# Kernel tuning notes

Hardware: AMD Instinct MI355X
Metric: run time of the kernel (lower is better)

Reference implementation:

```python
import jax, jax.numpy as jnp
import numpy as np

N_DATA = 128      # number of datasets (process conditions)
SEG_LEN = 131072  # thickness points per dataset
N_MAT = 8         # number of distinct materials
N_MATP = 8        # material params: Sigma0, BetaD, Ea, Mfda, Di, A0, B0, l0
N_PROCP = 5       # process params: SigmaC, K0, alpha1, L0, GrainSize_200
RGAS = 8.314      # gas constant, J/(mol K)


def setup_inputs() -> dict:
    key = jax.random.key(0)
    k1, k2, k3, k4 = jax.random.split(key, 4)
    # thickness points: sorted within each dataset segment, scaled to [0, 1]
    x = jax.random.uniform(k1, (N_DATA, SEG_LEN), dtype=jnp.float32)
    x_scaled = jnp.sort(x, axis=1).reshape(-1)
    # process conditions [R, T, P, Melting_T]
    pc = jax.random.uniform(k2, (N_DATA, 4), dtype=jnp.float32)
    R = 0.05 + pc[:, 0]            # deposition rate
    T = 300.0 + 300.0 * pc[:, 1]   # temperature (K)
    P = 0.1 + pc[:, 2]             # pressure
    material_index = jnp.sort(jax.random.randint(k3, (N_DATA,), 0, N_MAT, dtype=jnp.int32))
    melting_T = 1000.0 + 100.0 * material_index.astype(jnp.float32)
    process_c = jnp.stack([R, T, P, melting_T], axis=1)
    # learned raw parameters (pre-sigmoid) and bounds
    n_params = N_MAT * N_MATP + N_DATA * N_PROCP  # 704
    raw_params = 0.5 * jax.random.normal(k4, (n_params,), dtype=jnp.float32)
    para_lb = jnp.full((n_params,), 0.1, dtype=jnp.float32)
    para_ub = jnp.full((n_params,), 2.0, dtype=jnp.float32)
    # MinMaxScaler surrogates: [x_data_min, x_data_max, y_data_min, y_data_max], feature_range=(0,1)
    scaler_params = jnp.array([0.5, 500.0, -50.0, 50.0], dtype=jnp.float32)
    fit_index = jnp.repeat(jnp.arange(1, N_DATA + 1, dtype=jnp.int32), SEG_LEN)
    return {
        'x_scaled': x_scaled, 'process_c': process_c, 'raw_params': raw_params,
        'para_lb': para_lb, 'para_ub': para_ub, 'scaler_params': scaler_params,
        'fit_index': fit_index, 'material_index': material_index,
    }


def _stress(tp, R, T, P, SigmaC, alpha1, L0, G200, Sigma0, BetaD, Ea, Mfda, Di, A0, B0, l0):
    """Kinetic stress equation (Chason-type). tp: [N, L-1]; params broadcast [N, 1]."""
    Lg = G200 * (tp / 200.0 + 1e-3) ** alpha1 + L0      # grain size evolution
    D = Di * jnp.exp(-Ea / (RGAS * T))                   # thermally activated diffusivity
    beta = BetaD * D / (R * Lg + 1e-9)                   # kinetic competition factor
    sigma_ss = (SigmaC - Mfda * P + (Sigma0 / Lg) * beta) / (1.0 + beta)
    return sigma_ss + A0 * jnp.exp(-tp / (B0 * l0 + 1e-9))  # steady-state + transient


def reference(x_scaled, process_c, raw_params, para_lb, para_ub, scaler_params,
              fit_index, material_index):
    n_data = process_c.shape[0]
    seg = x_scaled.shape[0] // n_data
    # unscale parameters: sigmoid -> [lb, ub]
    xv = jax.nn.sigmoid(raw_params) * (para_ub - para_lb) + para_lb
    materials = xv[:N_MAT * N_MATP].reshape(N_MAT, N_MATP)
    process = xv[N_MAT * N_MATP:].reshape(n_data, N_PROCP)
    x_min, x_max, y_min, y_max = scaler_params[0], scaler_params[1], scaler_params[2], scaler_params[3]
    # inverse MinMax transform of thickness (feature_range = (0, 1))
    t = (x_scaled * (x_max - x_min) + x_min).reshape(n_data, seg)  # [N, L]
    SigmaC, K0, alpha1, L0, G200 = (process[:, i:i + 1] for i in range(5))
    mat = materials[material_index]  # [N, 8] gather per-dataset material params
    Sigma0, BetaD, Ea, Mfda, Di, A0, B0, l0 = (mat[:, i:i + 1] for i in range(8))
    R, T, P = process_c[:, 0:1], process_c[:, 1:2], process_c[:, 2:3]
    # Euler integration: Fit[j+1] = Fit[j] + stress(t[j]) * dT  ==  K0 + cumsum
    s = _stress(t[:, :-1], R, T, P, SigmaC, alpha1, L0, G200,
                Sigma0, BetaD, Ea, Mfda, Di, A0, B0, l0)   # [N, L-1]
    dT = jnp.diff(t, axis=1)                                # [N, L-1]
    fit = jnp.concatenate([K0, K0 + jnp.cumsum(s * dT, axis=1)], axis=1).reshape(-1)
    # forward MinMax transform of stress-thickness (feature_range = (0, 1))
    return (fit - y_min) / (y_max - y_min)
```

## Files before the change

kernel.cpp:

```cpp
#include <hip/hip_runtime.h>

#define N_DATA   128
#define SEG_LEN  131072
#define NPROD    (SEG_LEN - 1)
#define N_MAT    8
#define N_MATP   8
#define N_PROCP  5
#define RGAS     8.314f

#define TPB      256
#define EPT      16
#define WCHUNK   (64 * EPT)
#define WPR      (SEG_LEN / WCHUNK)
#define NWAVE    (N_DATA * WPR)
#define NBLK     (NWAVE / (TPB / 64))

typedef float nt4 __attribute__((ext_vector_type(4)));

__device__ __forceinline__ float stress_s(float t,
    float alpha1, float L0, float G200, float Sigma0, float A0,
    float inv_tau, float cbd, float base_num, float R) {
  float Lg  = G200 * __expf(alpha1 * __logf(t * (1.0f / 200.0f) + 0.001f)) + L0;
  float u   = R * Lg + 1e-9f;
  float num = base_num * u * Lg + Sigma0 * cbd;
  float den = Lg * (u + cbd);
  float sigma_ss = num * __builtin_amdgcn_rcpf(den);
  return sigma_ss + A0 * __expf(-t * inv_tau);
}

__global__ __launch_bounds__(TPB) void k0_init(unsigned long long* __restrict__ cs) {
  cs[blockIdx.x * TPB + threadIdx.x] = 0ull;
}

__global__ __launch_bounds__(TPB) void k_scan(
    const float* __restrict__ x,
    const float* __restrict__ pc, const float* __restrict__ raw,
    const float* __restrict__ lb, const float* __restrict__ ub,
    const float* __restrict__ sc, const int* __restrict__ mat_idx,
    unsigned long long* __restrict__ cs,
    float* __restrict__ out) {
  int tid  = threadIdx.x;
  int lane = tid & 63;
  int w    = blockIdx.x * (TPB >> 6) + (tid >> 6);
  int row  = __builtin_amdgcn_readfirstlane(w >> 7);
  int s    = w & (WPR - 1);

  long rowbase = (long)row * SEG_LEN;
  int  gbl = s * WCHUNK + lane * EPT;
  const float* xp = x + rowbase + gbl;
  float4 a0 = *(const float4*)(xp);
  float4 a1 = *(const float4*)(xp + 4);
  float4 a2 = *(const float4*)(xp + 8);
  float4 a3 = *(const float4*)(xp + 12);
  float  xn = (gbl + EPT < SEG_LEN) ? xp[EPT] : 0.0f;

  float pvl = 0.0f;
  if (lane < 13) {
    int idx = (lane < 5) ? (N_MAT * N_MATP + row * N_PROCP + lane)
                         : (mat_idx[row] * N_MATP + (lane - 5));
    float sg = 1.0f / (1.0f + __expf(-raw[idx]));
    pvl = sg * (ub[idx] - lb[idx]) + lb[idx];
  }
  float SigmaC = __shfl(pvl, 0),  K0   = __shfl(pvl, 1), alpha1 = __shfl(pvl, 2);
  float L0     = __shfl(pvl, 3),  G200 = __shfl(pvl, 4);
  float Sigma0 = __shfl(pvl, 5),  BetaD = __shfl(pvl, 6), Ea = __shfl(pvl, 7);
  float Mfda   = __shfl(pvl, 8),  Di   = __shfl(pvl, 9);
  float A0     = __shfl(pvl, 10), B0   = __shfl(pvl, 11), l0 = __shfl(pvl, 12);

  float R = pc[row * 4 + 0], T = pc[row * 4 + 1], P = pc[row * 4 + 2];
  float cbd      = BetaD * Di * __expf(-Ea / (RGAS * T));
  float base_num = SigmaC - Mfda * P;
  float inv_tau  = 1.0f / (B0 * l0 + 1e-9f);
  float x_min = sc[0], x_sc = sc[1] - sc[0];
  float y_min = sc[2], inv_yr = 1.0f / (sc[3] - sc[2]);

  float xr[EPT + 1];
  xr[0]=a0.x; xr[1]=a0.y; xr[2]=a0.z; xr[3]=a0.w;
  xr[4]=a1.x; xr[5]=a1.y; xr[6]=a1.z; xr[7]=a1.w;
  xr[8]=a2.x; xr[9]=a2.y; xr[10]=a2.z; xr[11]=a2.w;
  xr[12]=a3.x; xr[13]=a3.y; xr[14]=a3.z; xr[15]=a3.w;
  xr[16]=xn;

  float pref[EPT];
  float run  = 0.0f;
  float tcur = xr[0] * x_sc + x_min;
#pragma unroll
  for (int k = 0; k < EPT; k++) {
    float tnext = xr[k + 1] * x_sc + x_min;
    float p = 0.0f;
    if (gbl + k < NPROD) {
      float ss = stress_s(tcur, alpha1, L0, G200, Sigma0, A0, inv_tau, cbd, base_num, R);
      p = ss * (tnext - tcur);
    }
    run += p;
    pref[k] = run;
    tcur = tnext;
  }

  float incl = run;
#pragma unroll
  for (int d = 1; d < 64; d <<= 1) {
    float n = __shfl_up(incl, d);
    if (lane >= d) incl += n;
  }

  if (lane == 63) {
    unsigned long long u = (1ull << 32) |
        (unsigned long long)__float_as_uint(incl);
    __hip_atomic_store(cs + w, u, __ATOMIC_RELAXED, __HIP_MEMORY_SCOPE_AGENT);
  }

  float v = 0.0f;
  for (int c = lane; c < s; c += 64) {
    const unsigned long long* p = cs + ((row << 7) + c);
    unsigned long long u;
    do {
      u = __hip_atomic_load(p, __ATOMIC_RELAXED, __HIP_MEMORY_SCOPE_AGENT);
    } while (!(unsigned)(u >> 32));
    v += __uint_as_float((unsigned)u);
  }
#pragma unroll
  for (int d = 32; d > 0; d >>= 1) v += __shfl_down(v, d);
  float choff = __shfl(v, 0);

  float base = K0 + choff + (incl - run);
  nt4 o0, o1, o2, o3;
  o0.x = (base            - y_min) * inv_yr;
  o0.y = (base + pref[0]  - y_min) * inv_yr;
  o0.z = (base + pref[1]  - y_min) * inv_yr;
  o0.w = (base + pref[2]  - y_min) * inv_yr;
  o1.x = (base + pref[3]  - y_min) * inv_yr;
  o1.y = (base + pref[4]  - y_min) * inv_yr;
  o1.z = (base + pref[5]  - y_min) * inv_yr;
  o1.w = (base + pref[6]  - y_min) * inv_yr;
  o2.x = (base + pref[7]  - y_min) * inv_yr;
  o2.y = (base + pref[8]  - y_min) * inv_yr;
  o2.z = (base + pref[9]  - y_min) * inv_yr;
  o2.w = (base + pref[10] - y_min) * inv_yr;
  o3.x = (base + pref[11] - y_min) * inv_yr;
  o3.y = (base + pref[12] - y_min) * inv_yr;
  o3.z = (base + pref[13] - y_min) * inv_yr;
  o3.w = (base + pref[14] - y_min) * inv_yr;
  nt4* op = (nt4*)(out + rowbase + gbl);
  __builtin_nontemporal_store(o0, op);
  __builtin_nontemporal_store(o1, op + 1);
  __builtin_nontemporal_store(o2, op + 2);
  __builtin_nontemporal_store(o3, op + 3);
}

extern "C" void kernel_launch(void* const* d_in, const int* in_sizes, int n_in,
                              void* d_out, int out_size, void* d_ws, size_t ws_size,
                              hipStream_t stream) {
  const float* x_scaled  = (const float*)d_in[0];
  const float* process_c = (const float*)d_in[1];
  const float* raw       = (const float*)d_in[2];
  const float* lb        = (const float*)d_in[3];
  const float* ub        = (const float*)d_in[4];
  const float* sc        = (const float*)d_in[5];
  const int*   mat_idx   = (const int*)d_in[7];
  float* out = (float*)d_out;
  unsigned long long* cs = (unsigned long long*)d_ws;

  k0_init<<<NWAVE / TPB, TPB, 0, stream>>>(cs);
  k_scan<<<NBLK, TPB, 0, stream>>>(
      x_scaled, process_c, raw, lb, ub, sc, mat_idx, cs, out);
}
```

Measured before the change: 203.1 us.

## Coalesce wave loads and publish chunk total before local scan

Each lane now reads four float4s strided by 256 floats, so every wave load instruction touches contiguous memory, where before each lane read 16 contiguous floats. Neighbour values come from cross-lane shuffles, and four separate wave scans rebuild the prefix order. The chunk total is found with an xor reduction and published before the local scans, so later waves can stop waiting sooner. Outputs are prepared before the lookback wait, and the spin loop now sleeps between polls. This adds more shuffle work and changes the order of float summation.

Measured after the change: 181.0 us. 10.9% less time.

```diff
diff --git a/kernel.cpp b/kernel.cpp
--- a/kernel.cpp
+++ b/kernel.cpp
@@ -43,16 +43,17 @@
   int lane = tid & 63;
   int w    = blockIdx.x * (TPB >> 6) + (tid >> 6);
   int row  = __builtin_amdgcn_readfirstlane(w >> 7);
-  int s    = w & (WPR - 1);
+  int s    = __builtin_amdgcn_readfirstlane(w & (WPR - 1));
 
   long rowbase = (long)row * SEG_LEN;
-  int  gbl = s * WCHUNK + lane * EPT;
-  const float* xp = x + rowbase + gbl;
-  float4 a0 = *(const float4*)(xp);
-  float4 a1 = *(const float4*)(xp + 4);
-  float4 a2 = *(const float4*)(xp + 8);
-  float4 a3 = *(const float4*)(xp + 12);
-  float  xn = (gbl + EPT < SEG_LEN) ? xp[EPT] : 0.0f;
+  int  gb0 = s * WCHUNK;
+  const float* xp = x + rowbase + gb0 + lane * 4;
+  float4 v0 = *(const float4*)(xp);
+  float4 v1 = *(const float4*)(xp + 256);
+  float4 v2 = *(const float4*)(xp + 512);
+  float4 v3 = *(const float4*)(xp + 768);
+  float  xe = 0.0f;
+  if (lane == 63 && gb0 + WCHUNK < SEG_LEN) xe = x[rowbase + gb0 + WCHUNK];
 
   float pvl = 0.0f;
   if (lane < 13) {
@@ -74,78 +75,113 @@
   float x_min = sc[0], x_sc = sc[1] - sc[0];
   float y_min = sc[2], inv_yr = 1.0f / (sc[3] - sc[2]);
 
-  float xr[EPT + 1];
-  xr[0]=a0.x; xr[1]=a0.y; xr[2]=a0.z; xr[3]=a0.w;
-  xr[4]=a1.x; xr[5]=a1.y; xr[6]=a1.z; xr[7]=a1.w;
-  xr[8]=a2.x; xr[9]=a2.y; xr[10]=a2.z; xr[11]=a2.w;
-  xr[12]=a3.x; xr[13]=a3.y; xr[14]=a3.z; xr[15]=a3.w;
-  xr[16]=xn;
-
-  float pref[EPT];
-  float run  = 0.0f;
-  float tcur = xr[0] * x_sc + x_min;
+  float t0[4] = {v0.x*x_sc+x_min, v0.y*x_sc+x_min, v0.z*x_sc+x_min, v0.w*x_sc+x_min};
+  float t1[4] = {v1.x*x_sc+x_min, v1.y*x_sc+x_min, v1.z*x_sc+x_min, v1.w*x_sc+x_min};
+  float t2[4] = {v2.x*x_sc+x_min, v2.y*x_sc+x_min, v2.z*x_sc+x_min, v2.w*x_sc+x_min};
+  float t3[4] = {v3.x*x_sc+x_min, v3.y*x_sc+x_min, v3.z*x_sc+x_min, v3.w*x_sc+x_min};
+
+  float d0 = __shfl_down(t0[0], 1);
+  float d1 = __shfl_down(t1[0], 1);
+  float d2 = __shfl_down(t2[0], 1);
+  float d3 = __shfl_down(t3[0], 1);
+  float b1 = __shfl(t1[0], 0);
+  float b2 = __shfl(t2[0], 0);
+  float b3 = __shfl(t3[0], 0);
+  float xet = xe * x_sc + x_min;
+  bool last = (lane == 63);
+  float n0 = last ? b1  : d0;
+  float n1 = last ? b2  : d1;
+  float n2 = last ? b3  : d2;
+  float n3 = last ? xet : d3;
+
+  int glb = gb0 + lane * 4;
+  float p0[4], p1[4], p2[4], p3[4];
+#define PROD(pd, td, nd, roff)                                              \
+  {                                                                         \
+    _Pragma("unroll")                                                       \
+    for (int k = 0; k < 4; k++) {                                           \
+      float tn = (k < 3) ? td[k + 1] : nd;                                  \
+      float pp = 0.0f;                                                      \
+      if (glb + (roff) + k < NPROD) {                                       \
+        float ss = stress_s(td[k], alpha1, L0, G200, Sigma0, A0,            \
+                            inv_tau, cbd, base_num, R);                     \
+        pp = ss * (tn - td[k]);                                             \
+      }                                                                     \
+      pd[k] = pp;                                                           \
+    }                                                                       \
+  }
+  PROD(p0, t0, n0, 0)
+  PROD(p1, t1, n1, 256)
+  PROD(p2, t2, n2, 512)
+  PROD(p3, t3, n3, 768)
+#undef PROD
+
+  float rs0 = p0[0]+p0[1]+p0[2]+p0[3];
+  float rs1 = p1[0]+p1[1]+p1[2]+p1[3];
+  float rs2 = p2[0]+p2[1]+p2[2]+p2[3];
+  float rs3 = p3[0]+p3[1]+p3[2]+p3[3];
+
+  float tot = rs0 + rs1 + rs2 + rs3;
 #pragma unroll
-  for (int k = 0; k < EPT; k++) {
-    float tnext = xr[k + 1] * x_sc + x_min;
-    float p = 0.0f;
-    if (gbl + k < NPROD) {
-      float ss = stress_s(tcur, alpha1, L0, G200, Sigma0, A0, inv_tau, cbd, base_num, R);
-      p = ss * (tnext - tcur);
-    }
-    run += p;
-    pref[k] = run;
-    tcur = tnext;
-  }
-
-  float incl = run;
-#pragma unroll
-  for (int d = 1; d < 64; d <<= 1) {
-    float n = __shfl_up(incl, d);
-    if (lane >= d) incl += n;
-  }
-
-  if (lane == 63) {
+  for (int d = 1; d < 64; d <<= 1) tot += __shfl_xor(tot, d);
+  if (lane == 0) {
     unsigned long long u = (1ull << 32) |
-        (unsigned long long)__float_as_uint(incl);
+        (unsigned long long)__float_as_uint(tot);
     __hip_atomic_store(cs + w, u, __ATOMIC_RELAXED, __HIP_MEMORY_SCOPE_AGENT);
   }
 
-  float v = 0.0f;
+  float carry = 0.0f, e0, e1, e2, e3;
+#define SCAN(rs, er)                                                        \
+  {                                                                         \
+    float inc = rs;                                                         \
+    _Pragma("unroll")                                                       \
+    for (int d = 1; d < 64; d <<= 1) {                                      \
+      float nn = __shfl_up(inc, d);                                         \
+      if (lane >= d) inc += nn;                                             \
+    }                                                                       \
+    er = carry + inc - rs;                                                  \
+    carry += __shfl(inc, 63);                                               \
+  }
+  SCAN(rs0, e0) SCAN(rs1, e1) SCAN(rs2, e2) SCAN(rs3, e3)
+#undef SCAN
+
+  nt4 o0, o1, o2, o3;
+#define PREP(od, er, pd)                                                    \
+  {                                                                         \
+    float c0 = K0 + (er)        - y_min;                                    \
+    float c1 = c0 + pd[0];                                                  \
+    float c2 = c1 + pd[1];                                                  \
+    float c3 = c2 + pd[2];                                                  \
+    od.x = c0 * inv_yr; od.y = c1 * inv_yr;                                 \
+    od.z = c2 * inv_yr; od.w = c3 * inv_yr;                                 \
+  }
+  PREP(o0, e0, p0) PREP(o1, e1, p1) PREP(o2, e2, p2) PREP(o3, e3, p3)
+#undef PREP
+
+  float vsum = 0.0f;
   for (int c = lane; c < s; c += 64) {
     const unsigned long long* p = cs + ((row << 7) + c);
-    unsigned long long u;
-    do {
+    unsigned long long u = __hip_atomic_load(p, __ATOMIC_RELAXED, __HIP_MEMORY_SCOPE_AGENT);
+    while (!(unsigned)(u >> 32)) {
+      __builtin_amdgcn_s_sleep(1);
       u = __hip_atomic_load(p, __ATOMIC_RELAXED, __HIP_MEMORY_SCOPE_AGENT);
-    } while (!(unsigned)(u >> 32));
-    v += __uint_as_float((unsigned)u);
+    }
+    vsum += __uint_as_float((unsigned)u);
   }
 #pragma unroll
-  for (int d = 32; d > 0; d >>= 1) v += __shfl_down(v, d);
-  float choff = __shfl(v, 0);
-
-  float base = K0 + choff + (incl - run);
-  nt4 o0, o1, o2, o3;
-  o0.x = (base            - y_min) * inv_yr;
-  o0.y = (base + pref[0]  - y_min) * inv_yr;
-  o0.z = (base + pref[1]  - y_min) * inv_yr;
-  o0.w = (base + pref[2]  - y_min) * inv_yr;
-  o1.x = (base + pref[3]  - y_min) * inv_yr;
-  o1.y = (base + pref[4]  - y_min) * inv_yr;
-  o1.z = (base + pref[5]  - y_min) * inv_yr;
-  o1.w = (base + pref[6]  - y_min) * inv_yr;
-  o2.x = (base + pref[7]  - y_min) * inv_yr;
-  o2.y = (base + pref[8]  - y_min) * inv_yr;
-  o2.z = (base + pref[9]  - y_min) * inv_yr;
-  o2.w = (base + pref[10] - y_min) * inv_yr;
-  o3.x = (base + pref[11] - y_min) * inv_yr;
-  o3.y = (base + pref[12] - y_min) * inv_yr;
-  o3.z = (base + pref[13] - y_min) * inv_yr;
-  o3.w = (base + pref[14] - y_min) * inv_yr;
-  nt4* op = (nt4*)(out + rowbase + gbl);
-  __builtin_nontemporal_store(o0, op);
-  __builtin_nontemporal_store(o1, op + 1);
-  __builtin_nontemporal_store(o2, op + 2);
-  __builtin_nontemporal_store(o3, op + 3);
+  for (int d = 32; d > 0; d >>= 1) vsum += __shfl_down(vsum, d);
+  float choff = __shfl(vsum, 0) * inv_yr;
+
+  o0.x += choff; o0.y += choff; o0.z += choff; o0.w += choff;
+  o1.x += choff; o1.y += choff; o1.z += choff; o1.w += choff;
+  o2.x += choff; o2.y += choff; o2.z += choff; o2.w += choff;
+  o3.x += choff; o3.y += choff; o3.z += choff; o3.w += choff;
+
+  float* ob = out + rowbase + gb0 + lane * 4;
+  __builtin_nontemporal_store(o0, (nt4*)(ob));
+  __builtin_nontemporal_store(o1, (nt4*)(ob + 256));
+  __builtin_nontemporal_store(o2, (nt4*)(ob + 512));
+  __builtin_nontemporal_store(o3, (nt4*)(ob + 768));
 }
 
 extern "C" void kernel_launch(void* const* d_in, const int* in_sizes, int n_in,
```

## Use per-row bitmask lookback and coalesced strided loads with 32 elements per lane

Applied to the files above, without the earlier changes.

Each wave now handles twice as many elements, loaded as coalesced float4 runs strided across lanes, with neighbour values obtained by shuffles instead of per-lane contiguous chunks. Cross-wave offsets move from a polled per-wave flag-plus-value word to a per-row 64-bit ready mask updated with fetch_or and a separate value array, so a wave polls one word, with a short sleep between polls. The intent is better load coalescing, fewer waves and cheaper lookback, at the cost of eight in-wave scans per wave and more contention on the shared mask atomic.

Result: slower. 502.8 us (+147.6%).

```diff
diff --git a/kernel.cpp b/kernel.cpp
--- a/kernel.cpp
+++ b/kernel.cpp
@@ -9,7 +9,8 @@
 #define RGAS     8.314f
 
 #define TPB      256
-#define EPT      16
+#define RUNS     8
+#define EPT      (RUNS * 4)
 #define WCHUNK   (64 * EPT)
 #define WPR      (SEG_LEN / WCHUNK)
 #define NWAVE    (N_DATA * WPR)
@@ -28,8 +29,8 @@
   return sigma_ss + A0 * __expf(-t * inv_tau);
 }
 
-__global__ __launch_bounds__(TPB) void k0_init(unsigned long long* __restrict__ cs) {
-  cs[blockIdx.x * TPB + threadIdx.x] = 0ull;
+__global__ __launch_bounds__(128) void k0_init(unsigned long long* __restrict__ mask) {
+  mask[threadIdx.x] = 0ull;
 }
 
 __global__ __launch_bounds__(TPB) void k_scan(
@@ -37,22 +38,22 @@
     const float* __restrict__ pc, const float* __restrict__ raw,
     const float* __restrict__ lb, const float* __restrict__ ub,
     const float* __restrict__ sc, const int* __restrict__ mat_idx,
-    unsigned long long* __restrict__ cs,
+    unsigned long long* __restrict__ mask, float* __restrict__ val,
     float* __restrict__ out) {
   int tid  = threadIdx.x;
   int lane = tid & 63;
   int w    = blockIdx.x * (TPB >> 6) + (tid >> 6);
-  int row  = __builtin_amdgcn_readfirstlane(w >> 7);
-  int s    = w & (WPR - 1);
+  int row  = __builtin_amdgcn_readfirstlane(w / WPR);
+  int s    = __builtin_amdgcn_readfirstlane(w & (WPR - 1));
 
   long rowbase = (long)row * SEG_LEN;
-  int  gbl = s * WCHUNK + lane * EPT;
-  const float* xp = x + rowbase + gbl;
-  float4 a0 = *(const float4*)(xp);
-  float4 a1 = *(const float4*)(xp + 4);
-  float4 a2 = *(const float4*)(xp + 8);
-  float4 a3 = *(const float4*)(xp + 12);
-  float  xn = (gbl + EPT < SEG_LEN) ? xp[EPT] : 0.0f;
+  int  gb0 = s * WCHUNK;
+  const float* xp = x + rowbase + gb0 + lane * 4;
+  float4 v[RUNS];
+#pragma unroll
+  for (int r = 0; r < RUNS; r++) v[r] = *(const float4*)(xp + r * 256);
+  float xe = 0.0f;
+  if (lane == 63 && gb0 + WCHUNK < SEG_LEN) xe = x[rowbase + gb0 + WCHUNK];
 
   float pvl = 0.0f;
   if (lane < 13) {
@@ -74,78 +75,110 @@
   float x_min = sc[0], x_sc = sc[1] - sc[0];
   float y_min = sc[2], inv_yr = 1.0f / (sc[3] - sc[2]);
 
-  float xr[EPT + 1];
-  xr[0]=a0.x; xr[1]=a0.y; xr[2]=a0.z; xr[3]=a0.w;
-  xr[4]=a1.x; xr[5]=a1.y; xr[6]=a1.z; xr[7]=a1.w;
-  xr[8]=a2.x; xr[9]=a2.y; xr[10]=a2.z; xr[11]=a2.w;
-  xr[12]=a3.x; xr[13]=a3.y; xr[14]=a3.z; xr[15]=a3.w;
-  xr[16]=xn;
-
-  float pref[EPT];
-  float run  = 0.0f;
-  float tcur = xr[0] * x_sc + x_min;
-#pragma unroll
-  for (int k = 0; k < EPT; k++) {
-    float tnext = xr[k + 1] * x_sc + x_min;
-    float p = 0.0f;
-    if (gbl + k < NPROD) {
-      float ss = stress_s(tcur, alpha1, L0, G200, Sigma0, A0, inv_tau, cbd, base_num, R);
-      p = ss * (tnext - tcur);
+  float t[RUNS][4];
+#pragma unroll
+  for (int r = 0; r < RUNS; r++) {
+    t[r][0] = v[r].x * x_sc + x_min;
+    t[r][1] = v[r].y * x_sc + x_min;
+    t[r][2] = v[r].z * x_sc + x_min;
+    t[r][3] = v[r].w * x_sc + x_min;
+  }
+
+  float nx[RUNS];
+  {
+    float dsh[RUNS], bc[RUNS];
+#pragma unroll
+    for (int r = 0; r < RUNS; r++) dsh[r] = __shfl_down(t[r][0], 1);
+#pragma unroll
+    for (int r = 0; r < RUNS - 1; r++) bc[r] = __shfl(t[r + 1][0], 0);
+    bc[RUNS - 1] = xe * x_sc + x_min;
+    bool last = (lane == 63);
+#pragma unroll
+    for (int r = 0; r < RUNS; r++) nx[r] = last ? bc[r] : dsh[r];
+  }
+
+  int glb = gb0 + lane * 4;
+  float rs[RUNS];
+#pragma unroll
+  for (int r = 0; r < RUNS; r++) {
+    float acc = 0.0f;
+#pragma unroll
+    for (int k = 0; k < 4; k++) {
+      float tn = (k < 3) ? t[r][k + 1] : nx[r];
+      float pp = 0.0f;
+      if (glb + r * 256 + k < NPROD) {
+        float ss = stress_s(t[r][k], alpha1, L0, G200, Sigma0, A0,
+                            inv_tau, cbd, base_num, R);
+        pp = ss * (tn - t[r][k]);
+      }
+      acc += pp;
+      t[r][k] = pp;
     }
-    run += p;
-    pref[k] = run;
-    tcur = tnext;
-  }
-
-  float incl = run;
-#pragma unroll
-  for (int d = 1; d < 64; d <<= 1) {
-    float n = __shfl_up(incl, d);
-    if (lane >= d) incl += n;
-  }
-
-  if (lane == 63) {
-    unsigned long long u = (1ull << 32) |
-        (unsigned long long)__float_as_uint(incl);
-    __hip_atomic_store(cs + w, u, __ATOMIC_RELAXED, __HIP_MEMORY_SCOPE_AGENT);
-  }
-
-  float v = 0.0f;
-  for (int c = lane; c < s; c += 64) {
-    const unsigned long long* p = cs + ((row << 7) + c);
-    unsigned long long u;
-    do {
-      u = __hip_atomic_load(p, __ATOMIC_RELAXED, __HIP_MEMORY_SCOPE_AGENT);
-    } while (!(unsigned)(u >> 32));
-    v += __uint_as_float((unsigned)u);
-  }
-#pragma unroll
-  for (int d = 32; d > 0; d >>= 1) v += __shfl_down(v, d);
-  float choff = __shfl(v, 0);
-
-  float base = K0 + choff + (incl - run);
-  nt4 o0, o1, o2, o3;
-  o0.x = (base            - y_min) * inv_yr;
-  o0.y = (base + pref[0]  - y_min) * inv_yr;
-  o0.z = (base + pref[1]  - y_min) * inv_yr;
-  o0.w = (base + pref[2]  - y_min) * inv_yr;
-  o1.x = (base + pref[3]  - y_min) * inv_yr;
-  o1.y = (base + pref[4]  - y_min) * inv_yr;
-  o1.z = (base + pref[5]  - y_min) * inv_yr;
-  o1.w = (base + pref[6]  - y_min) * inv_yr;
-  o2.x = (base + pref[7]  - y_min) * inv_yr;
-  o2.y = (base + pref[8]  - y_min) * inv_yr;
-  o2.z = (base + pref[9]  - y_min) * inv_yr;
-  o2.w = (base + pref[10] - y_min) * inv_yr;
-  o3.x = (base + pref[11] - y_min) * inv_yr;
-  o3.y = (base + pref[12] - y_min) * inv_yr;
-  o3.z = (base + pref[13] - y_min) * inv_yr;
-  o3.w = (base + pref[14] - y_min) * inv_yr;
-  nt4* op = (nt4*)(out + rowbase + gbl);
-  __builtin_nontemporal_store(o0, op);
-  __builtin_nontemporal_store(o1, op + 1);
-  __builtin_nontemporal_store(o2, op + 2);
-  __builtin_nontemporal_store(o3, op + 3);
+    rs[r] = acc;
+  }
+
+  float tot = rs[0] + rs[1] + rs[2] + rs[3] + rs[4] + rs[5] + rs[6] + rs[7];
+#pragma unroll
+  for (int d = 1; d < 64; d <<= 1) tot += __shfl_xor(tot, d);
+  if (lane == 0) {
+    __hip_atomic_store(val + ((row << 6) + s), tot,
+                       __ATOMIC_RELAXED, __HIP_MEMORY_SCOPE_AGENT);
+    __hip_atomic_fetch_or(mask + row, 1ull << s,
+                          __ATOMIC_RELEASE, __HIP_MEMORY_SCOPE_AGENT);
+  }
+
+  float e[RUNS];
+  float carry = 0.0f;
+#pragma unroll
+  for (int r = 0; r < RUNS; r++) {
+    float inc = rs[r];
+#pragma unroll
+    for (int d = 1; d < 64; d <<= 1) {
+      float nn = __shfl_up(inc, d);
+      if (lane >= d) inc += nn;
+    }
+    e[r] = carry + inc - rs[r];
+    carry += __shfl(inc, 63);
+  }
+
+#pragma unroll
+  for (int r = 0; r < RUNS; r++) {
+    float c0 = K0 + e[r] - y_min;
+    float c1 = c0 + t[r][0];
+    float c2 = c1 + t[r][1];
+    float c3 = c2 + t[r][2];
+    t[r][0] = c0 * inv_yr; t[r][1] = c1 * inv_yr;
+    t[r][2] = c2 * inv_yr; t[r][3] = c3 * inv_yr;
+  }
+
+  float choff = 0.0f;
+  if (s > 0) {
+    unsigned long long need = (1ull << s) - 1ull;
+    const unsigned long long* mp = mask + row;
+    unsigned long long m = __hip_atomic_load(mp, __ATOMIC_RELAXED,
+                                             __HIP_MEMORY_SCOPE_AGENT);
+    while ((m & need) != need) {
+      __builtin_amdgcn_s_sleep(2);
+      m = __hip_atomic_load(mp, __ATOMIC_RELAXED, __HIP_MEMORY_SCOPE_AGENT);
+    }
+    __builtin_amdgcn_fence(__ATOMIC_ACQUIRE, "agent");
+    float vv = 0.0f;
+    if (lane < s)
+      vv = __hip_atomic_load(val + ((row << 6) + lane),
+                             __ATOMIC_RELAXED, __HIP_MEMORY_SCOPE_AGENT);
+#pragma unroll
+    for (int d = 32; d > 0; d >>= 1) vv += __shfl_down(vv, d);
+    choff = __shfl(vv, 0) * inv_yr;
+  }
+
+  float* ob = out + rowbase + gb0 + lane * 4;
+#pragma unroll
+  for (int r = 0; r < RUNS; r++) {
+    nt4 o;
+    o.x = t[r][0] + choff; o.y = t[r][1] + choff;
+    o.z = t[r][2] + choff; o.w = t[r][3] + choff;
+    __builtin_nontemporal_store(o, (nt4*)(ob + r * 256));
+  }
 }
 
 extern "C" void kernel_launch(void* const* d_in, const int* in_sizes, int n_in,
@@ -159,9 +192,10 @@
   const float* sc        = (const float*)d_in[5];
   const int*   mat_idx   = (const int*)d_in[7];
   float* out = (float*)d_out;
-  unsigned long long* cs = (unsigned long long*)d_ws;
-
-  k0_init<<<NWAVE / TPB, TPB, 0, stream>>>(cs);
+  unsigned long long* mask = (unsigned long long*)d_ws;
+  float* val = (float*)(mask + N_DATA);
+
+  k0_init<<<1, N_DATA, 0, stream>>>(mask);
   k_scan<<<NBLK, TPB, 0, stream>>>(
-      x_scaled, process_c, raw, lb, ub, sc, mat_idx, cs, out);
-}
+      x_scaled, process_c, raw, lb, ub, sc, mat_idx, mask, val, out);
+}
```

## Make scan waves persistent over four rows with double-buffered prefetch and coalesced tiles

Applied to the files above, without the earlier changes.

Each wave now handles a 2048-element chunk in four rows, loading the next row's tile and parameters while it computes the current one (register double-buffering). The per-lane layout moves from 16 contiguous elements to strided float4 runs, which keeps loads coalesced, and a multi-pass shuffle scan replaces the single one. Lookback now reads at most 63 predecessor slots per wave with one load each and sleeps while waiting. The goal is to hide memory latency and cut launch and lookback overhead, at the cost of more registers, lower occupancy and more shuffle work.

After: 171.8 us. 1.18x faster.

```diff
diff --git a/kernel.cpp b/kernel.cpp
--- a/kernel.cpp
+++ b/kernel.cpp
@@ -9,28 +9,173 @@
 #define RGAS     8.314f
 
 #define TPB      256
-#define EPT      16
-#define WCHUNK   (64 * EPT)
-#define WPR      (SEG_LEN / WCHUNK)
-#define NWAVE    (N_DATA * WPR)
-#define NBLK     (NWAVE / (TPB / 64))
+#define RUNS     8
+#define WCHUNK   (64 * RUNS * 4)
+#define SPR      (SEG_LEN / WCHUNK)
+#define NITER    4
+#define RPI      (N_DATA / NITER)
+#define NWAVEP   (RPI * SPR)
+#define NBLK     (NWAVEP / (TPB / 64))
+#define NSLOT    (N_DATA * SPR)
 
 typedef float nt4 __attribute__((ext_vector_type(4)));
-
-__device__ __forceinline__ float stress_s(float t,
-    float alpha1, float L0, float G200, float Sigma0, float A0,
-    float inv_tau, float cbd, float base_num, float R) {
-  float Lg  = G200 * __expf(alpha1 * __logf(t * (1.0f / 200.0f) + 0.001f)) + L0;
-  float u   = R * Lg + 1e-9f;
-  float num = base_num * u * Lg + Sigma0 * cbd;
-  float den = Lg * (u + cbd);
-  float sigma_ss = num * __builtin_amdgcn_rcpf(den);
-  return sigma_ss + A0 * __expf(-t * inv_tau);
-}
 
 __global__ __launch_bounds__(TPB) void k0_init(unsigned long long* __restrict__ cs) {
   cs[blockIdx.x * TPB + threadIdx.x] = 0ull;
 }
+
+__device__ __forceinline__ void load_tile(const float* __restrict__ x,
+    long rowbase, int gb0, int lane, float4 v[RUNS], float& xe) {
+  const float* xb = x + rowbase + gb0;
+  const float* xp = xb + lane * 4;
+#pragma unroll
+  for (int r = 0; r < RUNS; r++) v[r] = *(const float4*)(xp + r * 256);
+  xe = 0.0f;
+  if (lane == 63 && gb0 + WCHUNK < SEG_LEN) xe = xb[WCHUNK];
+}
+
+__device__ __forceinline__ void load_par(int row, int lane,
+    const float* __restrict__ raw, const float* __restrict__ lb,
+    const float* __restrict__ ub, const float* __restrict__ pc,
+    const int* __restrict__ mat_idx, float& pr, float& pl, float& pu) {
+  pr = 0.0f; pl = 0.0f; pu = 0.0f;
+  if (lane < 13) {
+    int idx = (lane < 5) ? (N_MAT * N_MATP + row * N_PROCP + lane)
+                         : (mat_idx[row] * N_MATP + (lane - 5));
+    pr = raw[idx]; pl = lb[idx]; pu = ub[idx];
+  } else if (lane < 16) {
+    pr = pc[row * 4 + (lane - 13)];
+  }
+}
+
+#define BODY(KK, VC, XEC, PRC, PLC, PUC, VN, XEN, PRN, PLN, PUN)             \
+  {                                                                          \
+    const int row = rb + RPI * (KK);                                         \
+    const long rowbase = (long)row * SEG_LEN;                                \
+    float pvl;                                                               \
+    if (lane < 13) {                                                         \
+      float sg = 1.0f / (1.0f + __expf(-(PRC)));                             \
+      pvl = sg * ((PUC) - (PLC)) + (PLC);                                    \
+    } else {                                                                 \
+      pvl = (PRC);                                                           \
+    }                                                                        \
+    float SigmaC = __shfl(pvl, 0),  Kzero = __shfl(pvl, 1);                  \
+    float alpha1 = __shfl(pvl, 2),  L0     = __shfl(pvl, 3);                 \
+    float G200   = __shfl(pvl, 4),  Sigma0 = __shfl(pvl, 5);                 \
+    float BetaD  = __shfl(pvl, 6),  Ea     = __shfl(pvl, 7);                 \
+    float Mfda   = __shfl(pvl, 8),  Di     = __shfl(pvl, 9);                 \
+    float A0     = __shfl(pvl, 10), B0     = __shfl(pvl, 11);                \
+    float l0     = __shfl(pvl, 12);                                          \
+    float R = __shfl(pvl, 13), T = __shfl(pvl, 14), P = __shfl(pvl, 15);     \
+    float cbd      = BetaD * Di * __expf(-Ea / (RGAS * T));                  \
+    float s0cbd    = Sigma0 * cbd;                                           \
+    float base_num = SigmaC - Mfda * P;                                      \
+    float inv_tau  = 1.0f / (B0 * l0 + 1e-9f);                               \
+    float t[RUNS][4];                                                        \
+    _Pragma("unroll")                                                        \
+    for (int r = 0; r < RUNS; r++) {                                         \
+      t[r][0] = VC[r].x * x_sc + x_min;                                      \
+      t[r][1] = VC[r].y * x_sc + x_min;                                      \
+      t[r][2] = VC[r].z * x_sc + x_min;                                      \
+      t[r][3] = VC[r].w * x_sc + x_min;                                      \
+    }                                                                        \
+    float nx[RUNS];                                                          \
+    {                                                                        \
+      float dsh[RUNS], bcx[RUNS];                                            \
+      _Pragma("unroll")                                                      \
+      for (int r = 0; r < RUNS; r++) dsh[r] = __shfl_down(t[r][0], 1);       \
+      _Pragma("unroll")                                                      \
+      for (int r = 0; r < RUNS - 1; r++) bcx[r] = __shfl(t[r + 1][0], 0);    \
+      bcx[RUNS - 1] = (XEC) * x_sc + x_min;    \
+      bool lastl = (lane == 63);                                             \
+      _Pragma("unroll")                                                      \
+      for (int r = 0; r < RUNS; r++) nx[r] = lastl ? bcx[r] : dsh[r];        \
+    }                                                                        \
+    int glb = gb0 + lane * 4;                                                \
+    float rs[RUNS];                                                          \
+    _Pragma("unroll")                                                        \
+    for (int r = 0; r < RUNS; r++) {                                         \
+      float acc = 0.0f;                                                      \
+      _Pragma("unroll")                                                      \
+      for (int kq = 0; kq < 4; kq++) {                                       \
+        float tn = (kq < 3) ? t[r][kq + 1] : nx[r];                          \
+        float pp = 0.0f;                                                     \
+        if (glb + r * 256 + kq < NPROD) {                                    \
+          float Lg = G200 * __expf(alpha1 *                                  \
+                       __logf(t[r][kq] * (1.0f / 200.0f) + 0.001f)) + L0;    \
+          float u  = R * Lg + 1e-9f;                                         \
+          float num = base_num * u * Lg + s0cbd;                             \
+          float den = Lg * (u + cbd);                                        \
+          float ss = num * __builtin_amdgcn_rcpf(den)                        \
+                   + A0 * __expf(-t[r][kq] * inv_tau);                       \
+          pp = ss * (tn - t[r][kq]);                                         \
+        }                                                                    \
+        acc += pp;                                                           \
+        t[r][kq] = pp;                             \
+      }                                                                      \
+      rs[r] = acc;                                                           \
+    }                                                                        \
+    float tot = rs[0]+rs[1]+rs[2]+rs[3]+rs[4]+rs[5]+rs[6]+rs[7];             \
+    _Pragma("unroll")                                                        \
+    for (int d = 1; d < 64; d <<= 1) tot += __shfl_xor(tot, d);              \
+    if (lane == 0) {                                                         \
+      unsigned long long u = (1ull << 32) |                                  \
+          (unsigned long long)__float_as_uint(tot);                          \
+      __hip_atomic_store(cs + ((row << 6) + s), u,                           \
+                         __ATOMIC_RELAXED, __HIP_MEMORY_SCOPE_AGENT);        \
+    }                                                                        \
+    if ((KK) + 1 < NITER) {         \
+      load_par(rb + RPI * ((KK) + 1), lane, raw, lb, ub, pc, mat_idx,        \
+               PRN, PLN, PUN);                                               \
+      load_tile(x, (long)(rb + RPI * ((KK) + 1)) * SEG_LEN, gb0, lane,       \
+                VN, XEN);                                                    \
+    }                                                                        \
+    float e[RUNS];                                                           \
+    float carry = 0.0f;                                                      \
+    _Pragma("unroll")                                                        \
+    for (int r = 0; r < RUNS; r++) {                                         \
+      float inc = rs[r];                                                     \
+      _Pragma("unroll")                                                      \
+      for (int d = 1; d < 64; d <<= 1) {                                     \
+        float nn = __shfl_up(inc, d);                                        \
+        if (lane >= d) inc += nn;                                            \
+      }                                                                      \
+      e[r] = carry + inc - rs[r];                                            \
+      carry += __shfl(inc, 63);                                              \
+    }                                                                        \
+    _Pragma("unroll")                                                        \
+    for (int r = 0; r < RUNS; r++) {                                         \
+      float c0 = Kzero + e[r] - y_min;                                       \
+      float c1 = c0 + t[r][0];                                               \
+      float c2 = c1 + t[r][1];                                               \
+      float c3 = c2 + t[r][2];                                               \
+      t[r][0] = c0 * inv_yr; t[r][1] = c1 * inv_yr;                          \
+      t[r][2] = c2 * inv_yr; t[r][3] = c3 * inv_yr;                          \
+    }                                                                        \
+    float vv = 0.0f;                                                         \
+    if (lane < s) {              \
+      const unsigned long long* p = cs + ((row << 6) + lane);                \
+      unsigned long long u = __hip_atomic_load(p, __ATOMIC_RELAXED,          \
+                                               __HIP_MEMORY_SCOPE_AGENT);    \
+      while (!(unsigned)(u >> 32)) {                                         \
+        __builtin_amdgcn_s_sleep(1);                                         \
+        u = __hip_atomic_load(p, __ATOMIC_RELAXED,                           \
+                              __HIP_MEMORY_SCOPE_AGENT);                     \
+      }                                                                      \
+      vv = __uint_as_float((unsigned)u);                                     \
+    }                                                                        \
+    _Pragma("unroll")                                                        \
+    for (int d = 32; d > 0; d >>= 1) vv += __shfl_down(vv, d);   \
+    float choff = __shfl(vv, 0) * inv_yr;         \
+    float* ob = out + rowbase + gb0 + lane * 4;                              \
+    _Pragma("unroll")                                                        \
+    for (int r = 0; r < RUNS; r++) {                                         \
+      nt4 o;                                                                 \
+      o.x = t[r][0] + choff; o.y = t[r][1] + choff;                          \
+      o.z = t[r][2] + choff; o.w = t[r][3] + choff;                          \
+      __builtin_nontemporal_store(o, (nt4*)(ob + r * 256));                  \
+    }                                                                        \
+  }
 
 __global__ __launch_bounds__(TPB) void k_scan(
     const float* __restrict__ x,
@@ -41,111 +186,25 @@
     float* __restrict__ out) {
   int tid  = threadIdx.x;
   int lane = tid & 63;
-  int w    = blockIdx.x * (TPB >> 6) + (tid >> 6);
-  int row  = __builtin_amdgcn_readfirstlane(w >> 7);
-  int s    = w & (WPR - 1);
-
-  long rowbase = (long)row * SEG_LEN;
-  int  gbl = s * WCHUNK + lane * EPT;
-  const float* xp = x + rowbase + gbl;
-  float4 a0 = *(const float4*)(xp);
-  float4 a1 = *(const float4*)(xp + 4);
-  float4 a2 = *(const float4*)(xp + 8);
-  float4 a3 = *(const float4*)(xp + 12);
-  float  xn = (gbl + EPT < SEG_LEN) ? xp[EPT] : 0.0f;
-
-  float pvl = 0.0f;
-  if (lane < 13) {
-    int idx = (lane < 5) ? (N_MAT * N_MATP + row * N_PROCP + lane)
-                         : (mat_idx[row] * N_MATP + (lane - 5));
-    float sg = 1.0f / (1.0f + __expf(-raw[idx]));
-    pvl = sg * (ub[idx] - lb[idx]) + lb[idx];
-  }
-  float SigmaC = __shfl(pvl, 0),  K0   = __shfl(pvl, 1), alpha1 = __shfl(pvl, 2);
-  float L0     = __shfl(pvl, 3),  G200 = __shfl(pvl, 4);
-  float Sigma0 = __shfl(pvl, 5),  BetaD = __shfl(pvl, 6), Ea = __shfl(pvl, 7);
-  float Mfda   = __shfl(pvl, 8),  Di   = __shfl(pvl, 9);
-  float A0     = __shfl(pvl, 10), B0   = __shfl(pvl, 11), l0 = __shfl(pvl, 12);
-
-  float R = pc[row * 4 + 0], T = pc[row * 4 + 1], P = pc[row * 4 + 2];
-  float cbd      = BetaD * Di * __expf(-Ea / (RGAS * T));
-  float base_num = SigmaC - Mfda * P;
-  float inv_tau  = 1.0f / (B0 * l0 + 1e-9f);
+  int W    = blockIdx.x * (TPB >> 6) + (tid >> 6);
+  int rb   = __builtin_amdgcn_readfirstlane(W >> 6);
+  int s    = __builtin_amdgcn_readfirstlane(W & (SPR - 1));
+  int gb0  = s * WCHUNK;
+
   float x_min = sc[0], x_sc = sc[1] - sc[0];
   float y_min = sc[2], inv_yr = 1.0f / (sc[3] - sc[2]);
 
-  float xr[EPT + 1];
-  xr[0]=a0.x; xr[1]=a0.y; xr[2]=a0.z; xr[3]=a0.w;
-  xr[4]=a1.x; xr[5]=a1.y; xr[6]=a1.z; xr[7]=a1.w;
-  xr[8]=a2.x; xr[9]=a2.y; xr[10]=a2.z; xr[11]=a2.w;
-  xr[12]=a3.x; xr[13]=a3.y; xr[14]=a3.z; xr[15]=a3.w;
-  xr[16]=xn;
-
-  float pref[EPT];
-  float run  = 0.0f;
-  float tcur = xr[0] * x_sc + x_min;
-#pragma unroll
-  for (int k = 0; k < EPT; k++) {
-    float tnext = xr[k + 1] * x_sc + x_min;
-    float p = 0.0f;
-    if (gbl + k < NPROD) {
-      float ss = stress_s(tcur, alpha1, L0, G200, Sigma0, A0, inv_tau, cbd, base_num, R);
-      p = ss * (tnext - tcur);
-    }
-    run += p;
-    pref[k] = run;
-    tcur = tnext;
-  }
-
-  float incl = run;
-#pragma unroll
-  for (int d = 1; d < 64; d <<= 1) {
-    float n = __shfl_up(incl, d);
-    if (lane >= d) incl += n;
-  }
-
-  if (lane == 63) {
-    unsigned long long u = (1ull << 32) |
-        (unsigned long long)__float_as_uint(incl);
-    __hip_atomic_store(cs + w, u, __ATOMIC_RELAXED, __HIP_MEMORY_SCOPE_AGENT);
-  }
-
-  float v = 0.0f;
-  for (int c = lane; c < s; c += 64) {
-    const unsigned long long* p = cs + ((row << 7) + c);
-    unsigned long long u;
-    do {
-      u = __hip_atomic_load(p, __ATOMIC_RELAXED, __HIP_MEMORY_SCOPE_AGENT);
-    } while (!(unsigned)(u >> 32));
-    v += __uint_as_float((unsigned)u);
-  }
-#pragma unroll
-  for (int d = 32; d > 0; d >>= 1) v += __shfl_down(v, d);
-  float choff = __shfl(v, 0);
-
-  float base = K0 + choff + (incl - run);
-  nt4 o0, o1, o2, o3;
-  o0.x = (base            - y_min) * inv_yr;
-  o0.y = (base + pref[0]  - y_min) * inv_yr;
-  o0.z = (base + pref[1]  - y_min) * inv_yr;
-  o0.w = (base + pref[2]  - y_min) * inv_yr;
-  o1.x = (base + pref[3]  - y_min) * inv_yr;
-  o1.y = (base + pref[4]  - y_min) * inv_yr;
-  o1.z = (base + pref[5]  - y_min) * inv_yr;
-  o1.w = (base + pref[6]  - y_min) * inv_yr;
-  o2.x = (base + pref[7]  - y_min) * inv_yr;
-  o2.y = (base + pref[8]  - y_min) * inv_yr;
-  o2.z = (base + pref[9]  - y_min) * inv_yr;
-  o2.w = (base + pref[10] - y_min) * inv_yr;
-  o3.x = (base + pref[11] - y_min) * inv_yr;
-  o3.y = (base + pref[12] - y_min) * inv_yr;
-  o3.z = (base + pref[13] - y_min) * inv_yr;
-  o3.w = (base + pref[14] - y_min) * inv_yr;
-  nt4* op = (nt4*)(out + rowbase + gbl);
-  __builtin_nontemporal_store(o0, op);
-  __builtin_nontemporal_store(o1, op + 1);
-  __builtin_nontemporal_store(o2, op + 2);
-  __builtin_nontemporal_store(o3, op + 3);
+  float4 vA[RUNS], vB[RUNS];
+  float xeA = 0.0f, xeB = 0.0f;
+  float prA, plA, puA, prB, plB, puB;
+
+  load_par(rb, lane, raw, lb, ub, pc, mat_idx, prA, plA, puA);
+  load_tile(x, (long)rb * SEG_LEN, gb0, lane, vA, xeA);
+
+  BODY(0, vA, xeA, prA, plA, puA, vB, xeB, prB, plB, puB)
+  BODY(1, vB, xeB, prB, plB, puB, vA, xeA, prA, plA, puA)
+  BODY(2, vA, xeA, prA, plA, puA, vB, xeB, prB, plB, puB)
+  BODY(3, vB, xeB, prB, plB, puB, vA, xeA, prA, plA, puA)
 }
 
 extern "C" void kernel_launch(void* const* d_in, const int* in_sizes, int n_in,
@@ -161,7 +220,7 @@
   float* out = (float*)d_out;
   unsigned long long* cs = (unsigned long long*)d_ws;
 
-  k0_init<<<NWAVE / TPB, TPB, 0, stream>>>(cs);
+  k0_init<<<NSLOT / TPB, TPB, 0, stream>>>(cs);
   k_scan<<<NBLK, TPB, 0, stream>>>(
       x_scaled, process_c, raw, lb, ub, sc, mat_idx, cs, out);
 }
```
